# Optimization experiments

Hardware: AMD Instinct MI355X
Metric: run time of the kernel (lower is better)

Reference implementation:

```python
import jax, jax.numpy as jnp
import numpy as np

R = 3          # routing iterations (init arg r)
EPS = 1e-7     # init arg epsilon


def squash(s, axis=-1):
    # squash(s) = ||s||^2 / (1 + ||s||^2) * s / (||s|| + EPS)
    n = jnp.linalg.norm(s, axis=axis, keepdims=True)
    n2 = jnp.square(n)
    return (n2 / (1.0 + n2)) * (s / (n + EPS))


def setup_inputs() -> dict:
    key = jax.random.key(0)
    k1, k2 = jax.random.split(key)
    B, S, P, J, I = 32, 32, 2048, 32, 16
    inputs = jax.random.normal(k1, (B, P, I), dtype=jnp.float32)
    # tf.random_normal_initializer default stddev = 0.05
    W = jax.random.normal(k2, (S, P, J, I), dtype=jnp.float32) * 0.05
    return {"inputs": inputs, "W": W}


def reference(inputs, W):
    # u_hat[b,s,p,j] = sum_i W[s,p,j,i] * inputs[b,p,i]
    u_hat = jnp.einsum('spji,bpi->bspj', W, inputs)  # [B,S,P,J]
    B, S, P, J = u_hat.shape
    b = jnp.zeros((B, S, 1, P), dtype=u_hat.dtype)
    v = None
    for _ in range(R):
        c = jax.nn.softmax(b, axis=-1)                     # over primary caps
        s = jnp.einsum('bsxp,bspj->bsxj', c, u_hat)        # [B,S,1,J]
        v = squash(s)                                      # [B,S,1,J]
        agreement = jnp.einsum('bsxj,bspj->bsxp', v, u_hat)  # [B,S,1,P]
        b = b + agreement
    return v.reshape(B, S, J)
```

## Files before the change

kernel.cpp:

```cpp
#include <hip/hip_runtime.h>
#include <stdint.h>

#define B_ 32
#define S_ 32
#define P_ 2048
#define J_ 32
#define I_ 16

#define UROW 16
#define UBSTRIDE ((size_t)S_ * P_ * UROW)

typedef _Float16 half8_t __attribute__((ext_vector_type(8)));
typedef float f32x16 __attribute__((ext_vector_type(16)));

__device__ inline float f16lo(uint32_t d) {
    return (float)__builtin_bit_cast(_Float16, (unsigned short)(d & 0xffffu));
}
__device__ inline float f16hi(uint32_t d) {
    return (float)__builtin_bit_cast(_Float16, (unsigned short)(d >> 16));
}

__global__ __launch_bounds__(256) void uhat_kernel(
        const float* __restrict__ W, const float* __restrict__ X,
        uint32_t* __restrict__ U) {
    const int tid  = threadIdx.x;
    const int lane = tid & 63;
    const int wave = tid >> 6;
    const int l31  = lane & 31;
    const int lhi  = lane >> 5;
    const int lpar = lane & 1;
    const int s    = blockIdx.y;
    const int p0   = blockIdx.x * 16 + wave * 4;

    __shared__ uint32_t xs[4][2048];

    float4 wv[4][2], xv[4][2];
    #pragma unroll
    for (int t = 0; t < 4; ++t) {
        const int p = p0 + t;
        const float* wr = W + (((size_t)s * P_ + p) * J_ + l31) * I_ + lhi * 8;
        wv[t][0] = *reinterpret_cast<const float4*>(wr);
        wv[t][1] = *reinterpret_cast<const float4*>(wr + 4);
        const float* xr = X + ((size_t)l31 * P_ + p) * I_ + lhi * 8;
        xv[t][0] = *reinterpret_cast<const float4*>(xr);
        xv[t][1] = *reinterpret_cast<const float4*>(xr + 4);
    }

    const int g  = l31 >> 1;
    const int gq = g >> 2, ge = g & 3;

    #pragma unroll
    for (int t = 0; t < 4; ++t) {
        half8_t A, Bf;
        A[0] = (_Float16)xv[t][0].x; A[1] = (_Float16)xv[t][0].y;
        A[2] = (_Float16)xv[t][0].z; A[3] = (_Float16)xv[t][0].w;
        A[4] = (_Float16)xv[t][1].x; A[5] = (_Float16)xv[t][1].y;
        A[6] = (_Float16)xv[t][1].z; A[7] = (_Float16)xv[t][1].w;
        Bf[0] = (_Float16)wv[t][0].x; Bf[1] = (_Float16)wv[t][0].y;
        Bf[2] = (_Float16)wv[t][0].z; Bf[3] = (_Float16)wv[t][0].w;
        Bf[4] = (_Float16)wv[t][1].x; Bf[5] = (_Float16)wv[t][1].y;
        Bf[6] = (_Float16)wv[t][1].z; Bf[7] = (_Float16)wv[t][1].w;

        f32x16 acc = {};
        acc = __builtin_amdgcn_mfma_f32_32x32x16_f16(A, Bf, acc, 0, 0, 0);

        #pragma unroll
        for (int m = 0; m < 8; ++m) {
            const int r = 2 * m;
            uint32_t lo16 = (uint32_t)__builtin_bit_cast(
                unsigned short, (_Float16)acc[r]);
            uint32_t hi16 = (uint32_t)__builtin_bit_cast(
                unsigned short, (_Float16)acc[r + 1]);
            uint32_t hp = lo16 | (hi16 << 16);
            uint32_t tp = (uint32_t)__shfl_xor((int)hp, 1, 64);
            uint32_t d = lpar ? ((tp >> 16) | (hp & 0xffff0000u))
                              : ((hp & 0xffffu) | (tp << 16));
            const int b = (r & 3) + lpar + 8 * (r >> 2) + 4 * lhi;
            const int k = (b >> 1) & 3;
            xs[wave][t * 512 + b * 16 + (((gq ^ k ^ t) & 3) << 2) + ge] = d;
        }
    }

    const int Lh  = lane >> 4;
    const int tr  = (lane >> 2) & 3;
    const int gqr = lane & 3;
    const int p   = p0 + tr;
    #pragma unroll
    for (int i = 0; i < 8; ++i) {
        const int b = 4 * i + Lh;
        const int k = (b >> 1) & 3;
        const int addr = tr * 512 + b * 16 + (((gqr ^ k ^ tr) & 3) << 2);
        uint4 vv = *reinterpret_cast<const uint4*>(&xs[wave][addr]);
        *reinterpret_cast<uint4*>(
            U + (size_t)b * UBSTRIDE + ((size_t)s * P_ + p) * UROW + 4 * gqr) = vv;
    }
}

template <int MASK, int HALF>
__device__ inline void red_level(float* red, int lane) {
    const bool hi = (lane & MASK) != 0;
    #pragma unroll
    for (int k = 0; k < HALF; ++k) {
        float send = hi ? red[k] : red[k + HALF];
        float recv = __shfl_xor(send, MASK, 64);
        red[k] = (hi ? red[k + HALF] : red[k]) + recv;
    }
}

__global__ __launch_bounds__(1024) void routing_kernel(
        const uint32_t* __restrict__ U, float* __restrict__ out) {
    const int tid  = threadIdx.x;
    const int lane = tid & 63;
    const int wid  = tid >> 6;
    const int bs   = blockIdx.x;

    __shared__ float sred[16 * 32];
    __shared__ float vlds[32];
    __shared__ float scal[32];

    const uint32_t* ub = U + (size_t)bs * ((size_t)P_ * UROW) + (size_t)tid * 32;
    uint32_t a[32];
    #pragma unroll
    for (int k = 0; k < 8; ++k) {
        uint4 t = reinterpret_cast<const uint4*>(ub)[k];
        a[k * 4 + 0] = t.x; a[k * 4 + 1] = t.y;
        a[k * 4 + 2] = t.z; a[k * 4 + 3] = t.w;
    }

    float bp0 = 0.0f, bp1 = 0.0f;

    for (int it = 0; it < 3; ++it) {
        float c0, c1;
        if (it == 0) {
            c0 = c1 = 1.0f / 2048.0f;
        } else {
            float mx = fmaxf(bp0, bp1);
            #pragma unroll
            for (int msk = 32; msk >= 1; msk >>= 1)
                mx = fmaxf(mx, __shfl_xor(mx, msk, 64));
            if (lane == 0) scal[wid] = mx;
            __syncthreads();
            mx = scal[0];
            #pragma unroll
            for (int w2 = 1; w2 < 16; ++w2) mx = fmaxf(mx, scal[w2]);
            float e0 = __expf(bp0 - mx);
            float e1 = __expf(bp1 - mx);
            float zs = e0 + e1;
            #pragma unroll
            for (int msk = 32; msk >= 1; msk >>= 1)
                zs += __shfl_xor(zs, msk, 64);
            if (lane == 0) scal[16 + wid] = zs;
            __syncthreads();
            float Z = 0.0f;
            #pragma unroll
            for (int w2 = 0; w2 < 16; ++w2) Z += scal[16 + w2];
            float invZ = 1.0f / Z;
            c0 = e0 * invZ;
            c1 = e1 * invZ;
        }

        float red[32];
        #pragma unroll
        for (int k = 0; k < 16; ++k) {
            uint32_t d0 = a[k], d1 = a[16 + k];
            red[2 * k]     = fmaf(c0, f16lo(d0), c1 * f16lo(d1));
            red[2 * k + 1] = fmaf(c0, f16hi(d0), c1 * f16hi(d1));
        }
        red_level<32, 16>(red, lane);
        red_level<16, 8>(red, lane);
        red_level<8, 4>(red, lane);
        red_level<4, 2>(red, lane);
        red_level<2, 1>(red, lane);
        red[0] += __shfl_xor(red[0], 1, 64);
        if ((lane & 1) == 0) sred[wid * 32 + (lane >> 1)] = red[0];
        __syncthreads();

        if (tid < 32) {
            float sv = 0.0f;
            #pragma unroll
            for (int w2 = 0; w2 < 16; ++w2) sv += sred[w2 * 32 + tid];
            float sq = sv * sv;
            #pragma unroll
            for (int msk = 16; msk >= 1; msk >>= 1)
                sq += __shfl_xor(sq, msk, 64);
            float n = sqrtf(sq);
            float scale = sq / ((1.0f + sq) * (n + 1e-7f));
            float v = sv * scale;
            vlds[tid] = v;
            if (it == 2) out[(size_t)bs * J_ + tid] = v;
        }
        __syncthreads();

        if (it < 2) {
            const float2* vl2 = reinterpret_cast<const float2*>(vlds);
            float ag0 = 0.0f, ag1 = 0.0f;
            #pragma unroll
            for (int k = 0; k < 16; ++k) {
                float2 vk = vl2[k];
                uint32_t d0 = a[k], d1 = a[16 + k];
                ag0 = fmaf(vk.x, f16lo(d0), ag0);
                ag0 = fmaf(vk.y, f16hi(d0), ag0);
                ag1 = fmaf(vk.x, f16lo(d1), ag1);
                ag1 = fmaf(vk.y, f16hi(d1), ag1);
            }
            bp0 += ag0;
            bp1 += ag1;
        }
    }
}

extern "C" void kernel_launch(void* const* d_in, const int* in_sizes, int n_in,
                              void* d_out, int out_size, void* d_ws, size_t ws_size,
                              hipStream_t stream) {
    (void)in_sizes; (void)n_in; (void)out_size;
    const float* X = (const float*)d_in[0];
    const float* W = (const float*)d_in[1];
    float* out     = (float*)d_out;
    uint32_t* U    = (uint32_t*)d_ws;

    const size_t need = (size_t)B_ * S_ * P_ * J_ * 2;
    if (ws_size < need) return;

    dim3 g1(P_ / 16, S_);
    uhat_kernel<<<g1, 256, 0, stream>>>(W, X, U);
    routing_kernel<<<B_ * S_, 1024, 0, stream>>>(U, out);
}
```

Before: 104.8 us.

## Reuse input fragments across 8 output capsules and prefetch W tiles

```diff
diff --git a/kernel.cpp b/kernel.cpp
--- a/kernel.cpp
+++ b/kernel.cpp
@@ -6,6 +6,7 @@
 #define P_ 2048
 #define J_ 32
 #define I_ 16
+#define STILE 8
 
 #define UROW 16
 #define UBSTRIDE ((size_t)S_ * P_ * UROW)
@@ -29,70 +30,89 @@
     const int l31  = lane & 31;
     const int lhi  = lane >> 5;
     const int lpar = lane & 1;
-    const int s    = blockIdx.y;
+    const int sb   = blockIdx.y * STILE;
     const int p0   = blockIdx.x * 16 + wave * 4;
 
     __shared__ uint32_t xs[4][2048];
 
-    float4 wv[4][2], xv[4][2];
+    half8_t xh[4];
     #pragma unroll
     for (int t = 0; t < 4; ++t) {
-        const int p = p0 + t;
-        const float* wr = W + (((size_t)s * P_ + p) * J_ + l31) * I_ + lhi * 8;
-        wv[t][0] = *reinterpret_cast<const float4*>(wr);
-        wv[t][1] = *reinterpret_cast<const float4*>(wr + 4);
-        const float* xr = X + ((size_t)l31 * P_ + p) * I_ + lhi * 8;
-        xv[t][0] = *reinterpret_cast<const float4*>(xr);
-        xv[t][1] = *reinterpret_cast<const float4*>(xr + 4);
-    }
-
-    const int g  = l31 >> 1;
-    const int gq = g >> 2, ge = g & 3;
-
-    #pragma unroll
-    for (int t = 0; t < 4; ++t) {
-        half8_t A, Bf;
-        A[0] = (_Float16)xv[t][0].x; A[1] = (_Float16)xv[t][0].y;
-        A[2] = (_Float16)xv[t][0].z; A[3] = (_Float16)xv[t][0].w;
-        A[4] = (_Float16)xv[t][1].x; A[5] = (_Float16)xv[t][1].y;
-        A[6] = (_Float16)xv[t][1].z; A[7] = (_Float16)xv[t][1].w;
-        Bf[0] = (_Float16)wv[t][0].x; Bf[1] = (_Float16)wv[t][0].y;
-        Bf[2] = (_Float16)wv[t][0].z; Bf[3] = (_Float16)wv[t][0].w;
-        Bf[4] = (_Float16)wv[t][1].x; Bf[5] = (_Float16)wv[t][1].y;
-        Bf[6] = (_Float16)wv[t][1].z; Bf[7] = (_Float16)wv[t][1].w;
-
-        f32x16 acc = {};
-        acc = __builtin_amdgcn_mfma_f32_32x32x16_f16(A, Bf, acc, 0, 0, 0);
-
-        #pragma unroll
-        for (int m = 0; m < 8; ++m) {
-            const int r = 2 * m;
-            uint32_t lo16 = (uint32_t)__builtin_bit_cast(
-                unsigned short, (_Float16)acc[r]);
-            uint32_t hi16 = (uint32_t)__builtin_bit_cast(
-                unsigned short, (_Float16)acc[r + 1]);
-            uint32_t hp = lo16 | (hi16 << 16);
-            uint32_t tp = (uint32_t)__shfl_xor((int)hp, 1, 64);
-            uint32_t d = lpar ? ((tp >> 16) | (hp & 0xffff0000u))
-                              : ((hp & 0xffffu) | (tp << 16));
-            const int b = (r & 3) + lpar + 8 * (r >> 2) + 4 * lhi;
-            const int k = (b >> 1) & 3;
-            xs[wave][t * 512 + b * 16 + (((gq ^ k ^ t) & 3) << 2) + ge] = d;
-        }
-    }
-
+        const float* xr = X + ((size_t)l31 * P_ + (p0 + t)) * I_ + lhi * 8;
+        float4 x0 = *reinterpret_cast<const float4*>(xr);
+        float4 x1 = *reinterpret_cast<const float4*>(xr + 4);
+        xh[t][0] = (_Float16)x0.x; xh[t][1] = (_Float16)x0.y;
+        xh[t][2] = (_Float16)x0.z; xh[t][3] = (_Float16)x0.w;
+        xh[t][4] = (_Float16)x1.x; xh[t][5] = (_Float16)x1.y;
+        xh[t][6] = (_Float16)x1.z; xh[t][7] = (_Float16)x1.w;
+    }
+
+    const int g   = l31 >> 1;
+    const int gq  = g >> 2, ge = g & 3;
     const int Lh  = lane >> 4;
     const int tr  = (lane >> 2) & 3;
     const int gqr = lane & 3;
-    const int p   = p0 + tr;
-    #pragma unroll
-    for (int i = 0; i < 8; ++i) {
-        const int b = 4 * i + Lh;
-        const int k = (b >> 1) & 3;
-        const int addr = tr * 512 + b * 16 + (((gqr ^ k ^ tr) & 3) << 2);
-        uint4 vv = *reinterpret_cast<const uint4*>(&xs[wave][addr]);
-        *reinterpret_cast<uint4*>(
-            U + (size_t)b * UBSTRIDE + ((size_t)s * P_ + p) * UROW + 4 * gqr) = vv;
+
+    float4 wv[2][4][2];
+    #pragma unroll
+    for (int t = 0; t < 4; ++t) {
+        const float* wr = W + (((size_t)sb * P_ + (p0 + t)) * J_ + l31) * I_ + lhi * 8;
+        wv[0][t][0] = *reinterpret_cast<const float4*>(wr);
+        wv[0][t][1] = *reinterpret_cast<const float4*>(wr + 4);
+    }
+
+    #pragma unroll
+    for (int ss = 0; ss < STILE; ++ss) {
+        const int cur = ss & 1, nxt = cur ^ 1;
+        if (ss + 1 < STILE) {
+            #pragma unroll
+            for (int t = 0; t < 4; ++t) {
+                const float* wr = W + (((size_t)(sb + ss + 1) * P_ + (p0 + t)) * J_
+                                        + l31) * I_ + lhi * 8;
+                wv[nxt][t][0] = *reinterpret_cast<const float4*>(wr);
+                wv[nxt][t][1] = *reinterpret_cast<const float4*>(wr + 4);
+            }
+        }
+        const int s = sb + ss;
+
+        #pragma unroll
+        for (int t = 0; t < 4; ++t) {
+            half8_t Bf;
+            Bf[0] = (_Float16)wv[cur][t][0].x; Bf[1] = (_Float16)wv[cur][t][0].y;
+            Bf[2] = (_Float16)wv[cur][t][0].z; Bf[3] = (_Float16)wv[cur][t][0].w;
+            Bf[4] = (_Float16)wv[cur][t][1].x; Bf[5] = (_Float16)wv[cur][t][1].y;
+            Bf[6] = (_Float16)wv[cur][t][1].z; Bf[7] = (_Float16)wv[cur][t][1].w;
+
+            f32x16 acc = {};
+            acc = __builtin_amdgcn_mfma_f32_32x32x16_f16(xh[t], Bf, acc, 0, 0, 0);
+
+            #pragma unroll
+            for (int m = 0; m < 8; ++m) {
+                const int r = 2 * m;
+                uint32_t lo16 = (uint32_t)__builtin_bit_cast(
+                    unsigned short, (_Float16)acc[r]);
+                uint32_t hi16 = (uint32_t)__builtin_bit_cast(
+                    unsigned short, (_Float16)acc[r + 1]);
+                uint32_t hp = lo16 | (hi16 << 16);
+                uint32_t tp = (uint32_t)__shfl_xor((int)hp, 1, 64);
+                uint32_t d = lpar ? ((tp >> 16) | (hp & 0xffff0000u))
+                                  : ((hp & 0xffffu) | (tp << 16));
+                const int b = (r & 3) + lpar + 8 * (r >> 2) + 4 * lhi;
+                const int k = (b >> 1) & 3;
+                xs[wave][t * 512 + b * 16 + (((gq ^ k ^ t) & 3) << 2) + ge] = d;
+            }
+        }
+
+        #pragma unroll
+        for (int i = 0; i < 8; ++i) {
+            const int b = 4 * i + Lh;
+            const int k = (b >> 1) & 3;
+            const int addr = tr * 512 + b * 16 + (((gqr ^ k ^ tr) & 3) << 2);
+            uint4 vv = *reinterpret_cast<const uint4*>(&xs[wave][addr]);
+            *reinterpret_cast<uint4*>(
+                U + (size_t)b * UBSTRIDE + ((size_t)s * P_ + (p0 + tr)) * UROW
+                  + 4 * gqr) = vv;
+        }
     }
 }
 
@@ -221,7 +241,7 @@
     const size_t need = (size_t)B_ * S_ * P_ * J_ * 2;
     if (ws_size < need) return;
 
-    dim3 g1(P_ / 16, S_);
+    dim3 g1(P_ / 16, S_ / STILE);
     uhat_kernel<<<g1, 256, 0, stream>>>(W, X, U);
     routing_kernel<<<B_ * S_, 1024, 0, stream>>>(U, out);
 }
```

After: 99.59 us. 1.05x faster.
